# Optimization experiments

Hardware: AMD Instinct MI355X
Metric: run time of the kernel (lower is better)

Reference implementation:

```python
import jax, jax.numpy as jnp
import numpy as np

B, L, D_MODEL = 4, 2048, 1024
D_INNER = 2 * D_MODEL
D_STATE, DT_RANK = 16, 64
Q = 32768.0  # 2^15 dyadic denominator used by the block


def _find_power_of_2_scale(var, eps=1e-9):
    v = var + eps
    scale = jnp.ones_like(v)
    for t, s in [(4.0, 0.5), (16.0, 0.25), (64.0, 0.125), (256.0, 0.0625),
                 (1024.0, 0.03125), (4096.0, 0.015625), (16384.0, 0.0078125),
                 (65536.0, 0.00390625)]:
        scale = jnp.where(v >= t, s, scale)
    scale = jnp.where(v < 1.0, 1.0, scale)
    scale = jnp.where(v < 0.25, 2.0, scale)
    scale = jnp.where(v < 0.0625, 4.0, scale)
    return scale


def _sigmoid_algebraic(z):
    return 0.5 + 0.5 * z / (1.0 + jnp.abs(z))


def _rsqrt_newton(y, num_iters=3):
    y = jnp.clip(y, 1e-6, 1e6)
    r = jnp.where(y > 16.0, 0.125, 0.5)
    r = jnp.where(y > 64.0, 0.0625, r)
    r = jnp.where(y > 256.0, 0.03125, r)
    r = jnp.where(y < 4.0, 1.0, r)
    r = jnp.where(y < 1.0, 2.0, r)
    r = jnp.where(y < 0.25, 4.0, r)
    for _ in range(num_iters):
        r = jnp.clip(r * (1.5 - 0.5 * y * r * r), 1e-6, 1e3)
    return r


def _squareplus(x):
    y = jnp.clip(x * x + 4.0, 1e-6, 1e6)
    s = jnp.clip(y * _rsqrt_newton(y), 0.0, 1e3)
    return 0.5 * (x + s)


def bitshift_norm(x, gamma, step_size):
    xc = x - x.mean(axis=-1, keepdims=True)
    var = (xc * xc).mean(axis=-1, keepdims=True)
    inv_disc = _find_power_of_2_scale(var)
    inv_diff = jax.lax.rsqrt(var + 1e-6)
    inv = inv_diff + jax.lax.stop_gradient(inv_disc - inv_diff)  # LSQ-style STE
    return xc * inv * gamma * step_size


def bitlinear(x, W):
    # 1.58-bit BitLinear: ternary weight quantization with STE
    s = jnp.mean(jnp.abs(W)) + 1e-8
    Wq = jnp.clip(jnp.round(W / s), -1.0, 1.0) * s
    Wq = W + jax.lax.stop_gradient(Wq - W)
    return x @ Wq.T


def dyadic_scan(u, decay):
    # h[t] = decay[t] * h[t-1] + (1 - decay[t]) * u[t]  (convex combination)
    a = decay
    b = (1.0 - decay) * u
    def comb(c1, c2):
        a1, b1 = c1
        a2, b2 = c2
        return a1 * a2, a2 * b1 + b2
    _, h = jax.lax.associative_scan(comb, (a, b), axis=1)
    return h


def setup_inputs() -> dict:
    key = jax.random.key(0)
    ks = jax.random.split(key, 9)
    d = {}
    d["x"] = jax.random.normal(ks[0], (B, L, D_MODEL), dtype=jnp.float32)
    d["gamma"] = jnp.ones((D_MODEL,), jnp.float32)
    d["step_size"] = jnp.ones((1,), jnp.float32)
    d["W_in"] = jax.random.normal(ks[1], (2 * D_INNER, D_MODEL), jnp.float32) * (D_MODEL ** -0.5)
    d["conv_w"] = jax.random.normal(ks[2], (D_INNER, 1, 4), jnp.float32) * 0.5
    d["conv_b"] = jnp.zeros((D_INNER,), jnp.float32)
    d["W_x"] = jax.random.normal(ks[3], (DT_RANK + 2 * D_STATE, D_INNER), jnp.float32) * (D_INNER ** -0.5)
    d["W_dt"] = jax.random.normal(ks[4], (D_INNER, DT_RANK), jnp.float32) * (DT_RANK ** -0.5)
    d["b_dt"] = jax.random.normal(ks[5], (D_INNER,), jnp.float32) * 0.1
    d["W_out"] = jax.random.normal(ks[6], (D_MODEL, D_INNER), jnp.float32) * (D_INNER ** -0.5)
    return d


def reference(x, gamma, step_size, W_in, conv_w, conv_b, W_x, W_dt, b_dt, W_out):
    Bc, Lc, _ = x.shape
    residual = x
    xn = bitshift_norm(x, gamma, step_size)
    xz = bitlinear(xn, W_in)                      # [B, L, 2*d_inner]
    xc, z = jnp.split(xz, 2, axis=-1)
    # causal depthwise conv1d (kernel 4, torch padding=3, slice back to L)
    xt = xc.transpose(0, 2, 1)                    # [B, d_inner, L]
    y = jax.lax.conv_general_dilated(
        xt, conv_w, (1,), [(3, 3)],
        dimension_numbers=("NCH", "OIH", "NCH"),
        feature_group_count=D_INNER)
    xc = (y[..., :Lc] + conv_b[None, :, None]).transpose(0, 2, 1)
    xc = _squareplus(xc)                          # integer-only activation
    dbl = bitlinear(xc, W_x)                      # [B, L, dt_rank + 2*d_state]
    dt = bitlinear(dbl[..., :DT_RANK], W_dt) + b_dt  # [B, L, d_inner]
    decay_c = _sigmoid_algebraic(dt)
    # dyadic quantization of decay to k/2^15 with STE
    decay = decay_c + jax.lax.stop_gradient(jnp.round(decay_c * Q) / Q - decay_c)
    h = dyadic_scan(xc, decay)                    # [B, L, d_inner]
    y = h * _squareplus(z)
    return bitlinear(y, W_out) + residual
```

## Files before the change

### kernel.cpp

```cpp
#include <hip/hip_runtime.h>
#include <hip/hip_bf16.h>

#define B_ 4
#define L_ 2048
#define DM 1024
#define DI 2048
#define NR (B_ * L_)
#define DTR 64
#define NCHUNK 16
#define CHUNK 128
#define KSLICE 8

typedef __attribute__((ext_vector_type(8))) short short8;
typedef __attribute__((ext_vector_type(4))) float floatx4;

static constexpr size_t OFF_SCAL = 0;
static constexpr size_t OFF_PART = 256;
static constexpr size_t OFF_XN   = 4608;
static constexpr size_t OFF_TIN  = OFF_XN   + (size_t)NR * DM * 2;
static constexpr size_t OFF_TX   = OFF_TIN  + (size_t)2 * DI * DM * 2;
static constexpr size_t OFF_TDT  = OFF_TX   + (size_t)DTR * DI * 2;
static constexpr size_t OFF_TOUT = OFF_TDT  + (size_t)DI * DTR * 2;
static constexpr size_t OFF_XC   = OFF_TOUT + (size_t)DM * DI * 2;
static constexpr size_t OFF_P2   = OFF_XC   + (size_t)NR * DI * 2;
static constexpr size_t OFF_ZSP  = OFF_XC   + (size_t)NR * DI * 4;
static constexpr size_t OFF_XACT = OFF_ZSP  + (size_t)NR * DI * 2;
static constexpr size_t OFF_DBL  = OFF_XACT + (size_t)NR * DI * 2;
static constexpr size_t OFF_DEC  = OFF_DBL  + (size_t)NR * DTR * 2;
static constexpr size_t OFF_CA   = OFF_DEC  + (size_t)NR * DI * 2;
static constexpr size_t OFF_CB   = OFF_CA   + (size_t)B_ * NCHUNK * DI * 4;
static constexpr size_t OFF_Y    = OFF_CB   + (size_t)B_ * NCHUNK * DI * 4;

__device__ __forceinline__ void async16(const void* g, void* l) {
    __builtin_amdgcn_global_load_lds(
        (const __attribute__((address_space(1))) unsigned int*)g,
        (__attribute__((address_space(3))) unsigned int*)l, 16, 0, 0);
}

__device__ __forceinline__ float pow2scale(float var) {
    float v = var + 1e-9f;
    float s = 1.0f;
    if (v >= 4.0f)     s = 0.5f;
    if (v >= 16.0f)    s = 0.25f;
    if (v >= 64.0f)    s = 0.125f;
    if (v >= 256.0f)   s = 0.0625f;
    if (v >= 1024.0f)  s = 0.03125f;
    if (v >= 4096.0f)  s = 0.015625f;
    if (v >= 16384.0f) s = 0.0078125f;
    if (v >= 65536.0f) s = 0.00390625f;
    if (v < 1.0f)    s = 1.0f;
    if (v < 0.25f)   s = 2.0f;
    if (v < 0.0625f) s = 4.0f;
    return s;
}

__device__ __forceinline__ float squareplus_f(float x) {
    float y = fminf(fmaxf(x * x + 4.0f, 1e-6f), 1e6f);
    float r = (y > 16.0f) ? 0.125f : 0.5f;
    if (y > 64.0f)  r = 0.0625f;
    if (y > 256.0f) r = 0.03125f;
    if (y < 4.0f)   r = 1.0f;
    if (y < 1.0f)   r = 2.0f;
    if (y < 0.25f)  r = 4.0f;
#pragma unroll
    for (int i = 0; i < 3; ++i) {
        r = r * (1.5f - 0.5f * y * r * r);
        r = fminf(fmaxf(r, 1e-6f), 1e3f);
    }
    float s = fminf(fmaxf(y * r, 0.0f), 1e3f);
    return 0.5f * (x + s);
}

__device__ __forceinline__ float block_reduce_sum(float v) {
    __shared__ float sm[4];
#pragma unroll
    for (int o = 32; o > 0; o >>= 1) v += __shfl_down(v, o, 64);
    int w = threadIdx.x >> 6;
    __syncthreads();
    if ((threadIdx.x & 63) == 0) sm[w] = v;
    __syncthreads();
    return (sm[0] + sm[1]) + (sm[2] + sm[3]);
}

__global__ __launch_bounds__(256) void k_abs_all(const float* __restrict__ W0,
                                                 const float* __restrict__ W1,
                                                 const float* __restrict__ W2,
                                                 const float* __restrict__ W3,
                                                 float* __restrict__ part) {
    const int w = blockIdx.y;
    const float* W = (w == 0) ? W0 : (w == 1) ? W1 : (w == 2) ? W2 : W3;
    const int n = (w == 0) ? 2 * DI * DM : (w == 1) ? 96 * DI : (w == 2) ? DI * DTR : DM * DI;
    float s = 0.f;
    for (int i = blockIdx.x * 256 + threadIdx.x; i < n; i += 256 * 256)
        s += fabsf(W[i]);
    float t = block_reduce_sum(s);
    if (threadIdx.x == 0) part[w * 256 + blockIdx.x] = t;
}

__global__ __launch_bounds__(256) void k_finalize(const float* __restrict__ part,
                                                  float* __restrict__ scal) {
    const float counts[4] = {(float)(2 * DI * DM), (float)(96 * DI),
                             (float)(DI * DTR), (float)(DM * DI)};
    for (int w = 0; w < 4; ++w) {
        float s = block_reduce_sum(part[w * 256 + threadIdx.x]);
        if (threadIdx.x == 0) scal[w] = s / counts[w] + 1e-8f;
    }
}

__global__ __launch_bounds__(256) void k_quant_all(
    const float* __restrict__ W0, const float* __restrict__ W1,
    const float* __restrict__ W2, const float* __restrict__ W3,
    const float* __restrict__ scal,
    __hip_bfloat16* __restrict__ T0, __hip_bfloat16* __restrict__ T1,
    __hip_bfloat16* __restrict__ T2, __hip_bfloat16* __restrict__ T3) {
    int b = blockIdx.x;
    const float* W; const float* sp; __hip_bfloat16* T; int off;
    if (b < 16384)      { W = W0; sp = scal + 0; T = T0; off = b; }
    else if (b < 16896) { W = W1; sp = scal + 1; T = T1; off = b - 16384; }
    else if (b < 17408) { W = W2; sp = scal + 2; T = T2; off = b - 16896; }
    else                { W = W3; sp = scal + 3; T = T3; off = b - 17408; }
    int i = off * 256 + threadIdx.x;
    float s = *sp;
    float q = rintf(W[i] / s);
    q = fmaxf(-1.0f, fminf(1.0f, q));
    T[i] = __float2bfloat16(q);
}

__global__ __launch_bounds__(256) void k_norm(const float* __restrict__ x,
                                              const float* __restrict__ gamma,
                                              const float* __restrict__ step,
                                              __hip_bfloat16* __restrict__ xn) {
    int row = blockIdx.x;
    const float* xr = x + (size_t)row * DM;
    float s = 0.f;
    for (int i = threadIdx.x; i < DM; i += 256) s += xr[i];
    float mean = block_reduce_sum(s) * (1.0f / DM);
    float v = 0.f;
    for (int i = threadIdx.x; i < DM; i += 256) { float d = xr[i] - mean; v += d * d; }
    float var = block_reduce_sum(v) * (1.0f / DM);
    float sc = pow2scale(var);
    float st = step[0];
    for (int i = threadIdx.x; i < DM; i += 256) {
        float val = ((xr[i] - mean) * sc) * gamma[i] * st;
        xn[(size_t)row * DM + i] = __float2bfloat16(val);
    }
}

template <int BM, int BN, int WR, int WC, int MODE>
__global__ __launch_bounds__(256) void k_gemm(
    const __hip_bfloat16* __restrict__ A, const __hip_bfloat16* __restrict__ Bw,
    int M, int N, int K, int lda, int ldb, const float* __restrict__ s_ptr,
    float* __restrict__ o_f32, __hip_bfloat16* __restrict__ o_bf16,
    __hip_bfloat16* __restrict__ o_bf16b, unsigned short* __restrict__ o_u16,
    const float* __restrict__ bias, const float* __restrict__ resid) {
    constexpr int BK = 32;
    constexpr int FM = BM / (WR * 16), FN = BN / (WC * 16);
    constexpr int RA = (BM * BK) / (256 * 8);
    constexpr int RB = (BN * BK) / (256 * 8);
    constexpr int KEEP = RA + RB;
    __shared__ __align__(16) short lA[3][BM * BK];
    __shared__ __align__(16) short lB[3][BN * BK];
    const int tid = threadIdx.x;
    const int lane = tid & 63, wid = tid >> 6;
    const int wm = (wid / WC) * (BM / WR);
    const int wn = (wid % WC) * (BN / WC);
    const int r16 = lane & 15, quad = lane >> 4;

    if (MODE == 4) {
        A  += (size_t)blockIdx.z * K;
        Bw += (size_t)blockIdx.z * K;
        o_f32 += (size_t)blockIdx.z * M * N;
    }

    int nx = gridDim.x;
    int bx = blockIdx.x, by = blockIdx.y;
    if ((nx & 7) == 0 && nx >= 8) {
        int bid = by * nx + bx;
        int xcd = bid & 7, idx = bid >> 3;
        int npx = nx >> 3;
        bx = xcd * npx + (idx % npx);
        by = idx / npx;
    }
    const int m0 = by * BM, n0 = bx * BN;

    floatx4 acc[FM][FN] = {};
    const int NT = K / BK;

#pragma unroll
    for (int r = 0; r < RA; ++r) {
        int idx = r * 256 + tid;
        int row = idx >> 2, kc = (idx & 3) << 3;
        async16(&A[(size_t)(m0 + row) * lda + kc], &lA[0][idx * 8]);
    }
#pragma unroll
    for (int r = 0; r < RB; ++r) {
        int idx = r * 256 + tid;
        int row = idx >> 2, kc = (idx & 3) << 3;
        async16(&Bw[(size_t)(n0 + row) * ldb + kc], &lB[0][idx * 8]);
    }
    if (NT > 1) {
#pragma unroll
        for (int r = 0; r < RA; ++r) {
            int idx = r * 256 + tid;
            int row = idx >> 2, kc = (idx & 3) << 3;
            async16(&A[(size_t)(m0 + row) * lda + BK + kc], &lA[1][idx * 8]);
        }
#pragma unroll
        for (int r = 0; r < RB; ++r) {
            int idx = r * 256 + tid;
            int row = idx >> 2, kc = (idx & 3) << 3;
            async16(&Bw[(size_t)(n0 + row) * ldb + BK + kc], &lB[1][idx * 8]);
        }
    }

    for (int t = 0; t < NT; ++t) {
        if (t > 0) __builtin_amdgcn_s_barrier();
        if (t + 2 < NT) {
            const int k2 = (t + 2) * BK;
            const int nb = (t + 2) % 3;
#pragma unroll
            for (int r = 0; r < RA; ++r) {
                int idx = r * 256 + tid;
                int row = idx >> 2, kc = (idx & 3) << 3;
                async16(&A[(size_t)(m0 + row) * lda + k2 + kc], &lA[nb][idx * 8]);
            }
#pragma unroll
            for (int r = 0; r < RB; ++r) {
                int idx = r * 256 + tid;
                int row = idx >> 2, kc = (idx & 3) << 3;
                async16(&Bw[(size_t)(n0 + row) * ldb + k2 + kc], &lB[nb][idx * 8]);
            }
            __builtin_amdgcn_s_waitcnt(0x0F70 | (2 * KEEP));
        } else if (t + 1 < NT) {
            __builtin_amdgcn_s_waitcnt(0x0F70 | KEEP);
        } else {
            __builtin_amdgcn_s_waitcnt(0x0F70);
        }
        __builtin_amdgcn_s_barrier();

        const int cb = t % 3;
        short8 af[FM], bfv[FN];
#pragma unroll
        for (int i = 0; i < FM; ++i)
            af[i] = *reinterpret_cast<const short8*>(&lA[cb][(wm + i * 16 + r16) * BK + quad * 8]);
#pragma unroll
        for (int j = 0; j < FN; ++j)
            bfv[j] = *reinterpret_cast<const short8*>(&lB[cb][(wn + j * 16 + r16) * BK + quad * 8]);
#pragma unroll
        for (int i = 0; i < FM; ++i)
#pragma unroll
            for (int j = 0; j < FN; ++j)
                acc[i][j] = __builtin_amdgcn_mfma_f32_16x16x32_bf16(af[i], bfv[j], acc[i][j], 0, 0, 0);
    }

    const float s = (MODE == 4) ? 1.0f : *s_ptr;
#pragma unroll
    for (int i = 0; i < FM; ++i) {
#pragma unroll
        for (int j = 0; j < FN; ++j) {
#pragma unroll
            for (int r = 0; r < 4; ++r) {
                int gr = m0 + wm + i * 16 + quad * 4 + r;
                int gc = n0 + wn + j * 16 + r16;
                float v = acc[i][j][r] * s;
                if (MODE == 0) {
                    if (gc < DI) o_bf16[(size_t)gr * DI + gc] = __float2bfloat16(v);
                    else o_bf16b[(size_t)gr * DI + (gc - DI)] = __float2bfloat16(v);
                } else if (MODE == 1) {
                    o_bf16[(size_t)gr * N + gc] = __float2bfloat16(v);
                } else if (MODE == 2) {
                    float dt = v + bias[gc];
                    float dc = 0.5f + 0.5f * dt / (1.0f + fabsf(dt));
                    o_u16[(size_t)gr * N + gc] = (unsigned short)rintf(dc * 32768.0f);
                } else if (MODE == 3) {
                    o_f32[(size_t)gr * N + gc] = v + resid[(size_t)gr * N + gc];
                } else {
                    o_f32[(size_t)gr * N + gc] = v;
                }
            }
        }
    }
}

__global__ __launch_bounds__(256) void k_red(const float* __restrict__ part,
                                             const float* __restrict__ s_ptr,
                                             __hip_bfloat16* __restrict__ dbl) {
    int i = blockIdx.x * 256 + threadIdx.x;
    float s = *s_ptr;
    float acc = 0.f;
#pragma unroll
    for (int z = 0; z < KSLICE; ++z) acc += part[(size_t)z * NR * DTR + i];
    dbl[i] = __float2bfloat16(acc * s);
}

__global__ __launch_bounds__(256) void k_conv(const __hip_bfloat16* __restrict__ xc,
                                              const float* __restrict__ cw,
                                              const float* __restrict__ cb,
                                              __hip_bfloat16* __restrict__ xact) {
    int c = blockIdx.x * 256 + threadIdx.x;
    int t0 = blockIdx.y * CHUNK;
    int b = blockIdx.z;
    float w0 = cw[c * 4 + 0], w1 = cw[c * 4 + 1], w2 = cw[c * 4 + 2], w3 = cw[c * 4 + 3];
    float bias = cb[c];
    const __hip_bfloat16* base = xc + (size_t)b * L_ * DI + c;
    float x3 = (t0 - 3 >= 0) ? __bfloat162float(base[(size_t)(t0 - 3) * DI]) : 0.f;
    float x2 = (t0 - 2 >= 0) ? __bfloat162float(base[(size_t)(t0 - 2) * DI]) : 0.f;
    float x1 = (t0 - 1 >= 0) ? __bfloat162float(base[(size_t)(t0 - 1) * DI]) : 0.f;
    for (int t = t0; t < t0 + CHUNK; ++t) {
        float xt = __bfloat162float(base[(size_t)t * DI]);
        float y = x3 * w0 + x2 * w1 + x1 * w2 + xt * w3 + bias;
        xact[((size_t)(b * L_ + t)) * DI + c] = __float2bfloat16(squareplus_f(y));
        x3 = x2; x2 = x1; x1 = xt;
    }
}

__global__ __launch_bounds__(256) void k_scan1(const unsigned short* __restrict__ dk,
                                               const __hip_bfloat16* __restrict__ u,
                                               float* __restrict__ cA, float* __restrict__ cB) {
    int c = blockIdx.x * 256 + threadIdx.x;
    int j = blockIdx.y, b = blockIdx.z;
    size_t base = ((size_t)b * L_ + (size_t)j * CHUNK) * DI + c;
    float Ac = 1.f, Bc = 0.f;
    for (int t = 0; t < CHUNK; ++t) {
        float a = dk[base + (size_t)t * DI] * (1.0f / 32768.0f);
        float uv = __bfloat162float(u[base + (size_t)t * DI]);
        Bc = a * Bc + (1.f - a) * uv;
        Ac *= a;
    }
    size_t o = ((size_t)(b * NCHUNK + j)) * DI + c;
    cA[o] = Ac;
    cB[o] = Bc;
}

__global__ __launch_bounds__(256) void k_scan3(const unsigned short* __restrict__ dk,
                                               const __hip_bfloat16* __restrict__ u,
                                               const __hip_bfloat16* __restrict__ zraw,
                                               const float* __restrict__ cA,
                                               const float* __restrict__ cB,
                                               __hip_bfloat16* __restrict__ y) {
    int c = blockIdx.x * 256 + threadIdx.x;
    int j = blockIdx.y, b = blockIdx.z;
    float h = 0.f;
    for (int jj = 0; jj < j; ++jj) {
        size_t o = ((size_t)(b * NCHUNK + jj)) * DI + c;
        h = cA[o] * h + cB[o];
    }
    size_t base = ((size_t)b * L_ + (size_t)j * CHUNK) * DI + c;
    for (int t = 0; t < CHUNK; ++t) {
        float a = dk[base + (size_t)t * DI] * (1.0f / 32768.0f);
        float uv = __bfloat162float(u[base + (size_t)t * DI]);
        h = a * h + (1.f - a) * uv;
        float zv = squareplus_f(__bfloat162float(zraw[base + (size_t)t * DI]));
        y[base + (size_t)t * DI] = __float2bfloat16(h * zv);
    }
}

extern "C" void kernel_launch(void* const* d_in, const int* in_sizes, int n_in,
                              void* d_out, int out_size, void* d_ws, size_t ws_size,
                              hipStream_t stream) {
    const float* x      = (const float*)d_in[0];
    const float* gamma  = (const float*)d_in[1];
    const float* step   = (const float*)d_in[2];
    const float* W_in   = (const float*)d_in[3];
    const float* conv_w = (const float*)d_in[4];
    const float* conv_b = (const float*)d_in[5];
    const float* W_x    = (const float*)d_in[6];
    const float* W_dt   = (const float*)d_in[7];
    const float* b_dt   = (const float*)d_in[8];
    const float* W_out  = (const float*)d_in[9];

    char* ws = (char*)d_ws;
    float*          scal = (float*)(ws + OFF_SCAL);
    float*          part = (float*)(ws + OFF_PART);
    __hip_bfloat16* xn   = (__hip_bfloat16*)(ws + OFF_XN);
    __hip_bfloat16* Tin  = (__hip_bfloat16*)(ws + OFF_TIN);
    __hip_bfloat16* Tx   = (__hip_bfloat16*)(ws + OFF_TX);
    __hip_bfloat16* Tdt  = (__hip_bfloat16*)(ws + OFF_TDT);
    __hip_bfloat16* Tout = (__hip_bfloat16*)(ws + OFF_TOUT);
    __hip_bfloat16* xcb  = (__hip_bfloat16*)(ws + OFF_XC);
    float*          p2   = (float*)(ws + OFF_P2);
    __hip_bfloat16* zraw = (__hip_bfloat16*)(ws + OFF_ZSP);
    __hip_bfloat16* xact = (__hip_bfloat16*)(ws + OFF_XACT);
    __hip_bfloat16* dbl  = (__hip_bfloat16*)(ws + OFF_DBL);
    unsigned short* dec  = (unsigned short*)(ws + OFF_DEC);
    float*          cA   = (float*)(ws + OFF_CA);
    float*          cB   = (float*)(ws + OFF_CB);
    __hip_bfloat16* yb   = (__hip_bfloat16*)(ws + OFF_Y);
    float*          out  = (float*)d_out;

    k_abs_all<<<dim3(256, 4), 256, 0, stream>>>(W_in, W_x, W_dt, W_out, part);
    k_finalize<<<1, 256, 0, stream>>>(part, scal);
    k_quant_all<<<25600, 256, 0, stream>>>(W_in, W_x, W_dt, W_out, scal, Tin, Tx, Tdt, Tout);

    k_norm<<<NR, 256, 0, stream>>>(x, gamma, step, xn);

    k_gemm<128, 128, 2, 2, 0><<<dim3((2 * DI) / 128, NR / 128), 256, 0, stream>>>(
        xn, Tin, NR, 2 * DI, DM, DM, DM, scal + 0, nullptr, xcb, zraw, nullptr, nullptr, nullptr);

    k_conv<<<dim3(DI / 256, L_ / CHUNK, B_), 256, 0, stream>>>(xcb, conv_w, conv_b, xact);

    k_gemm<64, 64, 2, 2, 4><<<dim3(1, NR / 64, KSLICE), 256, 0, stream>>>(
        xact, Tx, NR, DTR, DI / KSLICE, DI, DI, nullptr, p2, nullptr, nullptr, nullptr, nullptr, nullptr);
    k_red<<<(NR * DTR) / 256, 256, 0, stream>>>(p2, scal + 1, dbl);

    k_gemm<128, 128, 2, 2, 2><<<dim3(DI / 128, NR / 128), 256, 0, stream>>>(
        dbl, Tdt, NR, DI, DTR, DTR, DTR, scal + 2, nullptr, nullptr, nullptr, dec, b_dt, nullptr);

    k_scan1<<<dim3(DI / 256, NCHUNK, B_), 256, 0, stream>>>(dec, xact, cA, cB);
    k_scan3<<<dim3(DI / 256, NCHUNK, B_), 256, 0, stream>>>(dec, xact, zraw, cA, cB, yb);

    k_gemm<128, 128, 2, 2, 3><<<dim3(DM / 128, NR / 128), 256, 0, stream>>>(
        yb, Tout, NR, DM, DI, DI, DI, scal + 3, out, nullptr, nullptr, nullptr, nullptr, x);

    (void)in_sizes; (void)n_in; (void)out_size; (void)ws_size;
}
```

Before: 416.8 us.

## Vectorize weight/norm kernels, shrink scan and conv chunks, retile output GEMM

Vectorizes the weight abs-sum, quantize and norm kernels with float4 loads and packed bf16 stores, and replaces a per-element divide with a multiply by the reciprocal. Halves the scan and conv chunk length so more blocks run concurrently on these latency-bound sequential loops. Shrinks the output GEMM tile from 128x128 to 64x128 to launch more workgroups. Smaller scan chunks make the cross-chunk carry step do more work, and multiplying by the reciprocal can round slightly differently from the original divide.

```diff
diff --git a/kernel.cpp b/kernel.cpp
--- a/kernel.cpp
+++ b/kernel.cpp
@@ -7,8 +7,9 @@
 #define DI 2048
 #define NR (B_ * L_)
 #define DTR 64
-#define NCHUNK 16
-#define CHUNK 128
+#define NCHUNK 32
+#define CHUNK 64
+#define CCONV 64
 #define KSLICE 8
 
 typedef __attribute__((ext_vector_type(8))) short short8;
@@ -89,10 +90,13 @@
                                                  float* __restrict__ part) {
     const int w = blockIdx.y;
     const float* W = (w == 0) ? W0 : (w == 1) ? W1 : (w == 2) ? W2 : W3;
-    const int n = (w == 0) ? 2 * DI * DM : (w == 1) ? 96 * DI : (w == 2) ? DI * DTR : DM * DI;
+    const int n4 = ((w == 0) ? 2 * DI * DM : (w == 1) ? 96 * DI : (w == 2) ? DI * DTR : DM * DI) / 4;
+    const float4* W4 = (const float4*)W;
     float s = 0.f;
-    for (int i = blockIdx.x * 256 + threadIdx.x; i < n; i += 256 * 256)
-        s += fabsf(W[i]);
+    for (int i = blockIdx.x * 256 + threadIdx.x; i < n4; i += 256 * 256) {
+        float4 v = W4[i];
+        s += fabsf(v.x) + fabsf(v.y) + fabsf(v.z) + fabsf(v.w);
+    }
     float t = block_reduce_sum(s);
     if (threadIdx.x == 0) part[w * 256 + blockIdx.x] = t;
 }
@@ -115,15 +119,19 @@
     __hip_bfloat16* __restrict__ T2, __hip_bfloat16* __restrict__ T3) {
     int b = blockIdx.x;
     const float* W; const float* sp; __hip_bfloat16* T; int off;
-    if (b < 16384)      { W = W0; sp = scal + 0; T = T0; off = b; }
-    else if (b < 16896) { W = W1; sp = scal + 1; T = T1; off = b - 16384; }
-    else if (b < 17408) { W = W2; sp = scal + 2; T = T2; off = b - 16896; }
-    else                { W = W3; sp = scal + 3; T = T3; off = b - 17408; }
-    int i = off * 256 + threadIdx.x;
-    float s = *sp;
-    float q = rintf(W[i] / s);
-    q = fmaxf(-1.0f, fminf(1.0f, q));
-    T[i] = __float2bfloat16(q);
+    if (b < 4096)      { W = W0; sp = scal + 0; T = T0; off = b; }
+    else if (b < 4224) { W = W1; sp = scal + 1; T = T1; off = b - 4096; }
+    else if (b < 4352) { W = W2; sp = scal + 2; T = T2; off = b - 4224; }
+    else               { W = W3; sp = scal + 3; T = T3; off = b - 4352; }
+    int i = off * 1024 + threadIdx.x * 4;
+    float inv = 1.0f / (*sp);
+    float4 v = *(const float4*)(W + i);
+    __hip_bfloat16 t[4];
+    t[0] = __float2bfloat16(fmaxf(-1.0f, fminf(1.0f, rintf(v.x * inv))));
+    t[1] = __float2bfloat16(fmaxf(-1.0f, fminf(1.0f, rintf(v.y * inv))));
+    t[2] = __float2bfloat16(fmaxf(-1.0f, fminf(1.0f, rintf(v.z * inv))));
+    t[3] = __float2bfloat16(fmaxf(-1.0f, fminf(1.0f, rintf(v.w * inv))));
+    *reinterpret_cast<uint2*>(&T[i]) = *reinterpret_cast<uint2*>(t);
 }
 
 __global__ __launch_bounds__(256) void k_norm(const float* __restrict__ x,
@@ -131,19 +139,21 @@
                                               const float* __restrict__ step,
                                               __hip_bfloat16* __restrict__ xn) {
     int row = blockIdx.x;
-    const float* xr = x + (size_t)row * DM;
-    float s = 0.f;
-    for (int i = threadIdx.x; i < DM; i += 256) s += xr[i];
+    int tid = threadIdx.x;
+    float4 v4 = ((const float4*)(x + (size_t)row * DM))[tid];
+    float s = (v4.x + v4.y) + (v4.z + v4.w);
     float mean = block_reduce_sum(s) * (1.0f / DM);
-    float v = 0.f;
-    for (int i = threadIdx.x; i < DM; i += 256) { float d = xr[i] - mean; v += d * d; }
-    float var = block_reduce_sum(v) * (1.0f / DM);
-    float sc = pow2scale(var);
-    float st = step[0];
-    for (int i = threadIdx.x; i < DM; i += 256) {
-        float val = ((xr[i] - mean) * sc) * gamma[i] * st;
-        xn[(size_t)row * DM + i] = __float2bfloat16(val);
-    }
+    float d0 = v4.x - mean, d1 = v4.y - mean, d2 = v4.z - mean, d3 = v4.w - mean;
+    float vv = d0 * d0 + d1 * d1 + d2 * d2 + d3 * d3;
+    float var = block_reduce_sum(vv) * (1.0f / DM);
+    float sc = pow2scale(var) * step[0];
+    float4 g = ((const float4*)gamma)[tid];
+    __hip_bfloat16 t[4];
+    t[0] = __float2bfloat16(d0 * sc * g.x);
+    t[1] = __float2bfloat16(d1 * sc * g.y);
+    t[2] = __float2bfloat16(d2 * sc * g.z);
+    t[3] = __float2bfloat16(d3 * sc * g.w);
+    *reinterpret_cast<uint2*>(&xn[(size_t)row * DM + tid * 4]) = *reinterpret_cast<uint2*>(t);
 }
 
 template <int BM, int BN, int WR, int WC, int MODE>
@@ -298,7 +308,7 @@
                                               const float* __restrict__ cb,
                                               __hip_bfloat16* __restrict__ xact) {
     int c = blockIdx.x * 256 + threadIdx.x;
-    int t0 = blockIdx.y * CHUNK;
+    int t0 = blockIdx.y * CCONV;
     int b = blockIdx.z;
     float w0 = cw[c * 4 + 0], w1 = cw[c * 4 + 1], w2 = cw[c * 4 + 2], w3 = cw[c * 4 + 3];
     float bias = cb[c];
@@ -306,7 +316,7 @@
     float x3 = (t0 - 3 >= 0) ? __bfloat162float(base[(size_t)(t0 - 3) * DI]) : 0.f;
     float x2 = (t0 - 2 >= 0) ? __bfloat162float(base[(size_t)(t0 - 2) * DI]) : 0.f;
     float x1 = (t0 - 1 >= 0) ? __bfloat162float(base[(size_t)(t0 - 1) * DI]) : 0.f;
-    for (int t = t0; t < t0 + CHUNK; ++t) {
+    for (int t = t0; t < t0 + CCONV; ++t) {
         float xt = __bfloat162float(base[(size_t)t * DI]);
         float y = x3 * w0 + x2 * w1 + x1 * w2 + xt * w3 + bias;
         xact[((size_t)(b * L_ + t)) * DI + c] = __float2bfloat16(squareplus_f(y));
@@ -390,14 +400,14 @@
 
     k_abs_all<<<dim3(256, 4), 256, 0, stream>>>(W_in, W_x, W_dt, W_out, part);
     k_finalize<<<1, 256, 0, stream>>>(part, scal);
-    k_quant_all<<<25600, 256, 0, stream>>>(W_in, W_x, W_dt, W_out, scal, Tin, Tx, Tdt, Tout);
+    k_quant_all<<<6400, 256, 0, stream>>>(W_in, W_x, W_dt, W_out, scal, Tin, Tx, Tdt, Tout);
 
     k_norm<<<NR, 256, 0, stream>>>(x, gamma, step, xn);
 
     k_gemm<128, 128, 2, 2, 0><<<dim3((2 * DI) / 128, NR / 128), 256, 0, stream>>>(
         xn, Tin, NR, 2 * DI, DM, DM, DM, scal + 0, nullptr, xcb, zraw, nullptr, nullptr, nullptr);
 
-    k_conv<<<dim3(DI / 256, L_ / CHUNK, B_), 256, 0, stream>>>(xcb, conv_w, conv_b, xact);
+    k_conv<<<dim3(DI / 256, L_ / CCONV, B_), 256, 0, stream>>>(xcb, conv_w, conv_b, xact);
 
     k_gemm<64, 64, 2, 2, 4><<<dim3(1, NR / 64, KSLICE), 256, 0, stream>>>(
         xact, Tx, NR, DTR, DI / KSLICE, DI, DI, nullptr, p2, nullptr, nullptr, nullptr, nullptr, nullptr);
@@ -409,7 +419,7 @@
     k_scan1<<<dim3(DI / 256, NCHUNK, B_), 256, 0, stream>>>(dec, xact, cA, cB);
     k_scan3<<<dim3(DI / 256, NCHUNK, B_), 256, 0, stream>>>(dec, xact, zraw, cA, cB, yb);
 
-    k_gemm<128, 128, 2, 2, 3><<<dim3(DM / 128, NR / 128), 256, 0, stream>>>(
+    k_gemm<64, 128, 2, 2, 3><<<dim3(DM / 128, NR / 64), 256, 0, stream>>>(
         yb, Tout, NR, DM, DI, DI, DI, scal + 3, out, nullptr, nullptr, nullptr, nullptr, x);
 
     (void)in_sizes; (void)n_in; (void)out_size; (void)ws_size;
```

New measurement: 377.0 us. 1.11x faster.
